# Kernel optimization log

Measured on AMD Instinct MI355X. Metric: run time of the kernel, lower is better.

The kernel has to match this reference:

```python
import jax, jax.numpy as jnp
import numpy as np

N_VOXELS = 1024
N_RAYS = 2048
SH_DEGREE = 2
N_SH = 9            # (sh_degree+1)^2 with degree-2 real SH basis (1+3+5 terms)
S = 8               # ray_samples_per_voxel
BG_COLOR = (0.0, 0.0, 0.0)
FAR_PLANE = 100.0
EARLY_STOP_T = 0.01 # transmittance early-termination threshold from the torch loop


def eval_sh_basis(degree, dirs):
    # dirs: [..., 3] -> [..., N_SH]
    x, y, z = dirs[..., 0], dirs[..., 1], dirs[..., 2]
    sh = [jnp.ones_like(x)]
    if degree >= 1:
        sh += [y, z, x]
    if degree >= 2:
        sh += [x * y, y * z, 3 * z ** 2 - 1, x * z, x ** 2 - y ** 2]
    if degree >= 3:
        sh += [y * (3 * x ** 2 - y ** 2), x * y * z, y * (5 * z ** 2 - 1),
               z * (5 * z ** 2 - 3), x * (5 * z ** 2 - 1), (x ** 2 - y ** 2) * z,
               x * (x ** 2 - 3 * y ** 2)]
    return jnp.stack(sh, axis=-1)


def setup_inputs() -> dict:
    key = jax.random.key(0)
    ks = jax.random.split(key, 6)
    positions = jax.random.uniform(ks[0], (N_VOXELS, 3), minval=-1.0, maxval=1.0)
    sizes = 0.05 + 0.15 * jax.random.uniform(ks[1], (N_VOXELS,))
    densities = jax.random.normal(ks[2], (N_VOXELS,))
    colors = 0.3 * jax.random.normal(ks[3], (N_VOXELS, 3 * N_SH))
    ray_origins = jnp.array([0.0, 0.0, -3.0]) + 0.1 * jax.random.normal(ks[4], (N_RAYS, 3))
    targets = jax.random.uniform(ks[5], (N_RAYS, 3), minval=-1.0, maxval=1.0)
    d = targets - ray_origins
    ray_directions = d / jnp.linalg.norm(d, axis=-1, keepdims=True)
    return {"positions": positions, "sizes": sizes, "densities": densities,
            "colors": colors, "ray_origins": ray_origins, "ray_directions": ray_directions}


def _forward(positions, sizes, densities, colors, ray_o, ray_d):
    B = ray_o.shape[0]
    N = positions.shape[0]
    # ---- AABB intersection for all (ray, voxel) pairs ----
    half = (sizes / 2.0)[:, None]                      # [N,1]
    bmin = positions - half                            # [N,3]
    bmax = positions + half
    inv_d = 1.0 / ray_d                                # [B,3]
    t0 = (bmin[None, :, :] - ray_o[:, None, :]) * inv_d[:, None, :]   # [B,N,3]
    t1 = (bmax[None, :, :] - ray_o[:, None, :]) * inv_d[:, None, :]
    t_near = jnp.max(jnp.minimum(t0, t1), axis=-1)     # [B,N]
    t_far = jnp.min(jnp.maximum(t0, t1), axis=-1)
    valid = (t_far > t_near) & (t_far > 0.0)
    # sanitize invalid entries so no inf/nan leaks into masked-out math
    tn = jnp.where(valid, t_near, 0.0)
    tf = jnp.where(valid, t_far, 1.0)

    # ---- per-ray SH color (rgb_samples is constant across samples: dirs = ray_d) ----
    sh = eval_sh_basis(SH_DEGREE, ray_d)               # [B,C]
    coeffs = colors.reshape(N, 3, N_SH)                # [N,3,C]
    rgb_vox = jax.nn.sigmoid(jnp.einsum('bc,nkc->bnk', sh, coeffs))   # [B,N,3]

    # ---- within-voxel alpha compositing (S samples, constant sigma per voxel) ----
    sigma = jnp.exp(densities)                         # [N], density_activation='exp'
    delta = (tf - tn) / S                              # [B,N]
    alpha = 1.0 - jnp.exp(-sigma[None, :] * delta)     # [B,N]
    base = 1.0 - alpha + 1e-8
    i = jnp.arange(S, dtype=jnp.float32)
    pw = base[..., None] ** i                          # [B,N,S] exclusive cumprod of (1-a)
    w = alpha[..., None] * pw                          # per-sample weights
    frac = i / (S - 1)                                 # linspace(t_near, t_far, S)
    t_s = tn[..., None] + (tf - tn)[..., None] * frac  # [B,N,S]
    ws = jnp.where(valid, jnp.sum(w, -1), 0.0)         # [B,N] weight_sum per voxel
    depth_vox = jnp.where(valid, jnp.sum(w * t_s, -1), 0.0)

    # ---- sort voxels per ray by entry distance (invalid -> end) ----
    key_t = jnp.where(valid, tn, jnp.inf)
    order = jnp.argsort(key_t, axis=-1)                # [B,N]
    ws_s = jnp.take_along_axis(ws, order, -1)
    dep_s = jnp.take_along_axis(depth_vox, order, -1)
    rgb_s = jnp.take_along_axis(rgb_vox, order[..., None], 1)

    # ---- sequential compositing across voxels (closed form, with early-stop mask) ----
    one_m = 1.0 - ws_s
    T_before = jnp.cumprod(
        jnp.concatenate([jnp.ones((B, 1), one_m.dtype), one_m[:, :-1]], -1), axis=-1)
    proc = (T_before >= EARLY_STOP_T).astype(one_m.dtype)  # voxels processed before break
    contrib = T_before * ws_s * proc                   # [B,N]
    rgb_acc = jnp.einsum('bn,bnk->bk', contrib, rgb_s) # [B,3]
    depth_acc = jnp.sum(T_before * proc * dep_s, -1)   # [B]
    weight_acc = jnp.sum(contrib, -1)                  # [B]
    T_final = jnp.prod(1.0 - ws_s * proc, -1)          # transmittance at break/end

    bg = jnp.asarray(BG_COLOR, dtype=rgb_acc.dtype)
    rgb_acc = rgb_acc + T_final[:, None] * bg
    has_hit = valid.any(-1)
    depth = jnp.where(has_hit, depth_acc, FAR_PLANE)[:, None]
    return rgb_acc, depth, weight_acc[:, None]


def reference(positions, sizes, densities, colors, ray_origins, ray_directions):
    return _forward(positions, sizes, densities, colors, ray_origins, ray_directions)
```

## Files before the change

kernel.cpp:

```cpp
#include <hip/hip_runtime.h>


#define BLOCK 256
#define VPT   4
#define CAP   128
#define EARLY_STOP 0.01f

__global__ __launch_bounds__(BLOCK) void voxel_raster(
    const float* __restrict__ positions, const float* __restrict__ sizes,
    const float* __restrict__ densities, const float* __restrict__ colors,
    const float* __restrict__ ray_o, const float* __restrict__ ray_d,
    float* __restrict__ out, int N, int B)
{
    const int b   = blockIdx.x;
    const int tid = threadIdx.x;

    __shared__ int cnt;
    __shared__ unsigned long long key[CAP];
    __shared__ float raw_ws[CAP], raw_dep[CAP], raw_r[CAP], raw_g[CAP], raw_b[CAP];
    __shared__ float s_ws[CAP],  s_dep[CAP],  s_r[CAP],  s_g[CAP],  s_b[CAP];

    if (tid == 0) cnt = 0;
    __syncthreads();

    const float ox = ray_o[b*3+0], oy = ray_o[b*3+1], oz = ray_o[b*3+2];
    const float dx = ray_d[b*3+0], dy = ray_d[b*3+1], dz = ray_d[b*3+2];
    const float ivx = 1.0f/dx, ivy = 1.0f/dy, ivz = 1.0f/dz;

    float sh[9];
    sh[0]=1.0f; sh[1]=dy; sh[2]=dz; sh[3]=dx;
    sh[4]=dx*dy; sh[5]=dy*dz; sh[6]=3.0f*dz*dz-1.0f; sh[7]=dx*dz; sh[8]=dx*dx-dy*dy;

    #pragma unroll
    for (int k = 0; k < VPT; ++k) {
        const int n = tid + k * BLOCK;
        const float half = sizes[n] * 0.5f;
        const float px = positions[n*3+0];
        const float py = positions[n*3+1];
        const float pz = positions[n*3+2];

        float a0 = (px - half - ox) * ivx, a1 = (px + half - ox) * ivx;
        float tn = fminf(a0, a1), tf = fmaxf(a0, a1);
        a0 = (py - half - oy) * ivy; a1 = (py + half - oy) * ivy;
        tn = fmaxf(tn, fminf(a0, a1)); tf = fminf(tf, fmaxf(a0, a1));
        a0 = (pz - half - oz) * ivz; a1 = (pz + half - oz) * ivz;
        tn = fmaxf(tn, fminf(a0, a1)); tf = fminf(tf, fmaxf(a0, a1));

        if ((tf > tn) && (tf > 0.0f)) {
            const float sigma = expf(densities[n]);
            const float dt    = tf - tn;
            const float alpha = 1.0f - expf(-sigma * dt * 0.125f);
            const float base  = 1.0f - alpha + 1e-8f;
            float pw = 1.0f, ws = 0.0f, dep = 0.0f;
            #pragma unroll
            for (int i = 0; i < 8; i++) {
                const float w  = alpha * pw;
                const float ts = tn + dt * ((float)i * (1.0f / 7.0f));
                ws  += w;
                dep += w * ts;
                pw  *= base;
            }
            float rgb[3];
            #pragma unroll
            for (int c3 = 0; c3 < 3; c3++) {
                float acc = 0.0f;
                #pragma unroll
                for (int c = 0; c < 9; c++)
                    acc += sh[c] * colors[n*27 + c3*9 + c];
                rgb[c3] = 1.0f / (1.0f + expf(-acc));
            }

            const int slot = atomicAdd(&cnt, 1);
            if (slot < CAP) {
                unsigned u = __float_as_uint(tn);
                u = (u & 0x80000000u) ? ~u : (u | 0x80000000u);
                key[slot]     = ((unsigned long long)u << 32) | (unsigned)n;
                raw_ws[slot]  = ws;
                raw_dep[slot] = dep;
                raw_r[slot]   = rgb[0];
                raw_g[slot]   = rgb[1];
                raw_b[slot]   = rgb[2];
            }
        }
    }
    __syncthreads();

    const int total = cnt;
    const int m = (total < CAP) ? total : CAP;

    if (tid < 64) {
        for (int l = tid; l < m; l += 64) {
            const unsigned long long kl = key[l];
            int rank = 0;
            for (int j = 0; j < m; ++j) rank += (key[j] < kl);
            s_ws[rank]  = raw_ws[l];
            s_dep[rank] = raw_dep[l];
            s_r[rank]   = raw_r[l];
            s_g[rank]   = raw_g[l];
            s_b[rank]   = raw_b[l];
        }
    }
    __syncthreads();

    if (tid < 64) {
        const int lane = tid;
        float ra = 0.f, ga = 0.f, ba = 0.f, da = 0.f, wa = 0.f;
        float Tc = 1.0f;
        for (int basei = 0; basei < m; basei += 64) {
            const int idx = basei + lane;
            float ws = 0.f, dep = 0.f, cr = 0.f, cg = 0.f, cb = 0.f;
            if (idx < m) {
                ws = s_ws[idx]; dep = s_dep[idx];
                cr = s_r[idx];  cg = s_g[idx];  cb = s_b[idx];
            }
            float p = 1.0f - ws;
            #pragma unroll
            for (int off = 1; off < 64; off <<= 1) {
                const float q = __shfl_up(p, off, 64);
                if (lane >= off) p *= q;
            }
            float excl = __shfl_up(p, 1, 64);
            if (lane == 0) excl = 1.0f;
            const float Tb   = Tc * excl;
            const float proc = (Tb >= EARLY_STOP) ? 1.0f : 0.0f;
            const float contrib = Tb * ws * proc;
            ra += contrib * cr;
            ga += contrib * cg;
            ba += contrib * cb;
            da += Tb * proc * dep;
            wa += contrib;
            Tc *= __shfl(p, 63, 64);
        }
        #pragma unroll
        for (int off = 32; off > 0; off >>= 1) {
            ra += __shfl_down(ra, off, 64);
            ga += __shfl_down(ga, off, 64);
            ba += __shfl_down(ba, off, 64);
            da += __shfl_down(da, off, 64);
            wa += __shfl_down(wa, off, 64);
        }
        if (lane == 0) {
            out[b*3+0] = ra;
            out[b*3+1] = ga;
            out[b*3+2] = ba;
            out[B*3+b] = (total > 0) ? da : 100.0f;
            out[B*4+b] = wa;
        }
    }
}

extern "C" void kernel_launch(void* const* d_in, const int* in_sizes, int n_in,
                              void* d_out, int out_size, void* d_ws, size_t ws_size,
                              hipStream_t stream) {
    const float* positions = (const float*)d_in[0];
    const float* sizes     = (const float*)d_in[1];
    const float* densities = (const float*)d_in[2];
    const float* colors    = (const float*)d_in[3];
    const float* ray_o     = (const float*)d_in[4];
    const float* ray_d     = (const float*)d_in[5];
    const int N = in_sizes[1];
    const int B = in_sizes[4] / 3;

    voxel_raster<<<B, BLOCK, 0, stream>>>(
        positions, sizes, densities, colors, ray_o, ray_d, (float*)d_out, N, B);
}
```

Baseline: 73.12 us.

## Replace rank sort and scan with per-hit direct transmittance products

```diff
diff --git a/kernel.cpp b/kernel.cpp
--- a/kernel.cpp
+++ b/kernel.cpp
@@ -2,7 +2,6 @@
 
 
 #define BLOCK 256
-#define VPT   4
 #define CAP   128
 #define EARLY_STOP 0.01f
 
@@ -10,15 +9,14 @@
     const float* __restrict__ positions, const float* __restrict__ sizes,
     const float* __restrict__ densities, const float* __restrict__ colors,
     const float* __restrict__ ray_o, const float* __restrict__ ray_d,
-    float* __restrict__ out, int N, int B)
+    float* __restrict__ out, int B)
 {
     const int b   = blockIdx.x;
     const int tid = threadIdx.x;
 
     __shared__ int cnt;
     __shared__ unsigned long long key[CAP];
-    __shared__ float raw_ws[CAP], raw_dep[CAP], raw_r[CAP], raw_g[CAP], raw_b[CAP];
-    __shared__ float s_ws[CAP],  s_dep[CAP],  s_r[CAP],  s_g[CAP],  s_b[CAP];
+    __shared__ float h_ws[CAP], h_dep[CAP], h_r[CAP], h_g[CAP], h_b[CAP];
 
     if (tid == 0) cnt = 0;
     __syncthreads();
@@ -31,13 +29,21 @@
     sh[0]=1.0f; sh[1]=dy; sh[2]=dz; sh[3]=dx;
     sh[4]=dx*dy; sh[5]=dy*dz; sh[6]=3.0f*dz*dz-1.0f; sh[7]=dx*dz; sh[8]=dx*dx-dy*dy;
 
+    const float4 P0 = ((const float4*)positions)[tid*3+0];
+    const float4 P1 = ((const float4*)positions)[tid*3+1];
+    const float4 P2 = ((const float4*)positions)[tid*3+2];
+    const float4 SZ = ((const float4*)sizes)[tid];
+
+    const float pxa[4] = {P0.x, P0.w, P1.z, P2.y};
+    const float pya[4] = {P0.y, P1.x, P1.w, P2.z};
+    const float pza[4] = {P0.z, P1.y, P2.x, P2.w};
+    const float hsa[4] = {SZ.x*0.5f, SZ.y*0.5f, SZ.z*0.5f, SZ.w*0.5f};
+
     #pragma unroll
-    for (int k = 0; k < VPT; ++k) {
-        const int n = tid + k * BLOCK;
-        const float half = sizes[n] * 0.5f;
-        const float px = positions[n*3+0];
-        const float py = positions[n*3+1];
-        const float pz = positions[n*3+2];
+    for (int k = 0; k < 4; ++k) {
+        const int n = tid*4 + k;
+        const float half = hsa[k];
+        const float px = pxa[k], py = pya[k], pz = pza[k];
 
         float a0 = (px - half - ox) * ivx, a1 = (px + half - ox) * ivx;
         float tn = fminf(a0, a1), tf = fmaxf(a0, a1);
@@ -47,9 +53,9 @@
         tn = fmaxf(tn, fminf(a0, a1)); tf = fminf(tf, fmaxf(a0, a1));
 
         if ((tf > tn) && (tf > 0.0f)) {
-            const float sigma = expf(densities[n]);
+            const float sigma = __expf(densities[n]);
             const float dt    = tf - tn;
-            const float alpha = 1.0f - expf(-sigma * dt * 0.125f);
+            const float alpha = 1.0f - __expf(-sigma * dt * 0.125f);
             const float base  = 1.0f - alpha + 1e-8f;
             float pw = 1.0f, ws = 0.0f, dep = 0.0f;
             #pragma unroll
@@ -67,19 +73,19 @@
                 #pragma unroll
                 for (int c = 0; c < 9; c++)
                     acc += sh[c] * colors[n*27 + c3*9 + c];
-                rgb[c3] = 1.0f / (1.0f + expf(-acc));
+                rgb[c3] = __fdividef(1.0f, 1.0f + __expf(-acc));
             }
 
             const int slot = atomicAdd(&cnt, 1);
             if (slot < CAP) {
                 unsigned u = __float_as_uint(tn);
                 u = (u & 0x80000000u) ? ~u : (u | 0x80000000u);
-                key[slot]     = ((unsigned long long)u << 32) | (unsigned)n;
-                raw_ws[slot]  = ws;
-                raw_dep[slot] = dep;
-                raw_r[slot]   = rgb[0];
-                raw_g[slot]   = rgb[1];
-                raw_b[slot]   = rgb[2];
+                key[slot]   = ((unsigned long long)u << 32) | (unsigned)n;
+                h_ws[slot]  = ws;
+                h_dep[slot] = dep;
+                h_r[slot]   = rgb[0];
+                h_g[slot]   = rgb[1];
+                h_b[slot]   = rgb[2];
             }
         }
     }
@@ -89,47 +95,24 @@
     const int m = (total < CAP) ? total : CAP;
 
     if (tid < 64) {
+        float ra = 0.f, ga = 0.f, ba = 0.f, da = 0.f, wa = 0.f;
         for (int l = tid; l < m; l += 64) {
             const unsigned long long kl = key[l];
-            int rank = 0;
-            for (int j = 0; j < m; ++j) rank += (key[j] < kl);
-            s_ws[rank]  = raw_ws[l];
-            s_dep[rank] = raw_dep[l];
-            s_r[rank]   = raw_r[l];
-            s_g[rank]   = raw_g[l];
-            s_b[rank]   = raw_b[l];
-        }
-    }
-    __syncthreads();
-
-    if (tid < 64) {
-        const int lane = tid;
-        float ra = 0.f, ga = 0.f, ba = 0.f, da = 0.f, wa = 0.f;
-        float Tc = 1.0f;
-        for (int basei = 0; basei < m; basei += 64) {
-            const int idx = basei + lane;
-            float ws = 0.f, dep = 0.f, cr = 0.f, cg = 0.f, cb = 0.f;
-            if (idx < m) {
-                ws = s_ws[idx]; dep = s_dep[idx];
-                cr = s_r[idx];  cg = s_g[idx];  cb = s_b[idx];
+            float Tb = 1.0f;
+            for (int j = 0; j < m; ++j) {
+                const unsigned long long kj = key[j];
+                const float wj = h_ws[j];
+                Tb *= (kj < kl) ? (1.0f - wj) : 1.0f;
             }
-            float p = 1.0f - ws;
-            #pragma unroll
-            for (int off = 1; off < 64; off <<= 1) {
-                const float q = __shfl_up(p, off, 64);
-                if (lane >= off) p *= q;
+            if (Tb >= EARLY_STOP) {
+                const float ws = h_ws[l];
+                const float c  = Tb * ws;
+                ra += c * h_r[l];
+                ga += c * h_g[l];
+                ba += c * h_b[l];
+                da += Tb * h_dep[l];
+                wa += c;
             }
-            float excl = __shfl_up(p, 1, 64);
-            if (lane == 0) excl = 1.0f;
-            const float Tb   = Tc * excl;
-            const float proc = (Tb >= EARLY_STOP) ? 1.0f : 0.0f;
-            const float contrib = Tb * ws * proc;
-            ra += contrib * cr;
-            ga += contrib * cg;
-            ba += contrib * cb;
-            da += Tb * proc * dep;
-            wa += contrib;
-            Tc *= __shfl(p, 63, 64);
         }
         #pragma unroll
         for (int off = 32; off > 0; off >>= 1) {
@@ -139,7 +122,7 @@
             da += __shfl_down(da, off, 64);
             wa += __shfl_down(wa, off, 64);
         }
-        if (lane == 0) {
+        if (tid == 0) {
             out[b*3+0] = ra;
             out[b*3+1] = ga;
             out[b*3+2] = ba;
@@ -158,9 +141,8 @@
     const float* colors    = (const float*)d_in[3];
     const float* ray_o     = (const float*)d_in[4];
     const float* ray_d     = (const float*)d_in[5];
-    const int N = in_sizes[1];
     const int B = in_sizes[4] / 3;
 
     voxel_raster<<<B, BLOCK, 0, stream>>>(
-        positions, sizes, densities, colors, ray_o, ray_d, (float*)d_out, N, B);
+        positions, sizes, densities, colors, ray_o, ray_d, (float*)d_out, B);
 }
```

Result: faster. 70.65 us (-3.4%).
